# Optimization experiments

Hardware: AMD Instinct MI355X
Metric: run time of the kernel (lower is better)

Reference implementation:

```python
import jax, jax.numpy as jnp
import numpy as np

NUM_PRIMARY_CAPS = 32
PRIMARY_CAP_DIM = 8
CLASS_CAP_DIM = 16
NUM_SLOTS = 100
ROUTING_ITERS = 3
PRIOR_STRENGTH = 0.1
PRIOR_DECAY = 0.02
TEMPERATURE_INIT = 30.0

INPUT_DIM = 20000
NUM_LABELS = 100
BATCH = 4096


def _layernorm(x, g, b, eps=1e-5):
    mu = x.mean(axis=-1, keepdims=True)
    var = x.var(axis=-1, keepdims=True)
    return (x - mu) / jnp.sqrt(var + eps) * g + b


def _squash(t, axis=-1):
    sq = (t ** 2).sum(axis=axis, keepdims=True)
    scale = sq / (1.0 + sq)
    return scale * t / jnp.sqrt(sq + 1e-8)


def _l2norm(x, axis=-1, eps=1e-12):
    n = jnp.sqrt((x ** 2).sum(axis=axis, keepdims=True))
    return x / jnp.maximum(n, eps)


def setup_inputs() -> dict:
    key = jax.random.key(0)
    ks = jax.random.split(key, 12)
    features = jax.random.normal(ks[0], (BATCH, INPUT_DIM), dtype=jnp.float32)
    features = _l2norm(features)  # L2-normalised TF-IDF per docstring
    slot_features = jax.random.normal(ks[1], (BATCH, NUM_SLOTS), dtype=jnp.float32)
    # embedding MLP: Linear(input_dim,512) ReLU Linear(512,256) ReLU LayerNorm(256)
    W1 = jax.random.normal(ks[2], (INPUT_DIM, 512), dtype=jnp.float32) * 0.02
    b1 = jnp.zeros((512,), jnp.float32)
    W2 = jax.random.normal(ks[3], (512, 256), dtype=jnp.float32) * 0.05
    b2 = jnp.zeros((256,), jnp.float32)
    ln_g = jnp.ones((256,), jnp.float32)
    ln_b = jnp.zeros((256,), jnp.float32)
    # primary caps: 32 independent Linear(256,8)+LayerNorm(8), stacked
    pc_W = jax.random.normal(ks[4], (NUM_PRIMARY_CAPS, 256, PRIMARY_CAP_DIM), dtype=jnp.float32) * 0.06
    pc_b = jnp.zeros((NUM_PRIMARY_CAPS, PRIMARY_CAP_DIM), jnp.float32)
    pc_g = jnp.ones((NUM_PRIMARY_CAPS, PRIMARY_CAP_DIM), jnp.float32)
    pc_beta = jnp.zeros((NUM_PRIMARY_CAPS, PRIMARY_CAP_DIM), jnp.float32)
    # digit caps routing weights [N, K, out, in] * 0.1 per torch init
    dc_W = jax.random.normal(ks[5], (NUM_PRIMARY_CAPS, NUM_LABELS, CLASS_CAP_DIM, PRIMARY_CAP_DIM), dtype=jnp.float32) * 0.1
    slot_priors = jax.random.normal(ks[6], (NUM_SLOTS, NUM_LABELS), dtype=jnp.float32) * 0.05
    targets = _l2norm(jax.random.normal(ks[7], (NUM_LABELS, CLASS_CAP_DIM), dtype=jnp.float32))
    temperature = jnp.asarray(TEMPERATURE_INIT, dtype=jnp.float32)
    return {"features": features, "slot_features": slot_features,
            "W1": W1, "b1": b1, "W2": W2, "b2": b2, "ln_g": ln_g, "ln_b": ln_b,
            "pc_W": pc_W, "pc_b": pc_b, "pc_g": pc_g, "pc_beta": pc_beta,
            "dc_W": dc_W, "slot_priors": slot_priors, "targets": targets,
            "temperature": temperature}


def reference(features, slot_features, W1, b1, W2, b2, ln_g, ln_b,
              pc_W, pc_b, pc_g, pc_beta, dc_W, slot_priors, targets, temperature):
    # embedding MLP (dropout is identity at inference)
    h = jax.nn.relu(features @ W1 + b1)
    h = jax.nn.relu(h @ W2 + b2)
    h = _layernorm(h, ln_g, ln_b)                      # [B, 256]
    # primary capsules: [B, N=32, 8]
    prim = jnp.einsum('bc,ncd->bnd', h, pc_W) + pc_b[None]
    prim = _layernorm(prim, pc_g[None], pc_beta[None])
    # routing predictions: [B, N, K, out]
    predictions = jnp.einsum('bni,njoi->bnjo', prim, dc_W)
    B = features.shape[0]
    # slot prior: relu -> normalize to simplex -> center -> project to classes
    sf_relu = jax.nn.relu(slot_features)
    sf_w = sf_relu / jnp.maximum(sf_relu.sum(axis=1, keepdims=True), 1e-6)
    sf_w = sf_w - 1.0 / NUM_SLOTS
    sp = (sf_w @ slot_priors)[:, None, :, None]        # [B, 1, K, 1]
    b = jnp.zeros((B, NUM_PRIMARY_CAPS, predictions.shape[2], 1), predictions.dtype)
    b = b + sp * PRIOR_STRENGTH
    v = None
    for i in range(ROUTING_ITERS):
        c = jax.nn.softmax(b, axis=2)                  # coupling coefficients
        s = (predictions * c).sum(axis=1, keepdims=True)
        v = _squash(s, axis=-1)                        # [B, 1, K, out]
        if i < ROUTING_ITERS - 1:
            b = b + (predictions * v).sum(axis=-1, keepdims=True)
            strength_i = max(0.0, PRIOR_STRENGTH - PRIOR_DECAY * (i + 1))
            b = b + sp * strength_i
    class_caps = v[:, 0]                               # [B, K, out]
    caps_n = _l2norm(class_caps)
    logits = (caps_n * targets[None]).sum(axis=-1) * temperature
    return logits
```

## Files before the change

### kernel.cpp

```cpp
#include <hip/hip_runtime.h>
#include <hip/hip_bf16.h>

#define B_SZ   4096
#define NPC    32
#define NJ     100
#define CD     16
#define PD     8

typedef float  f32x4  __attribute__((ext_vector_type(4)));
typedef __bf16 bf16x8 __attribute__((ext_vector_type(8)));

__device__ __forceinline__ unsigned short f2bfr(float f) {
    union { float f; unsigned u; } v; v.f = f;
    return (unsigned short)((v.u + 0x8000u) >> 16);
}
__device__ __forceinline__ float bf_lo(unsigned u) {
    union { unsigned u; float f; } v; v.u = u << 16; return v.f;
}
__device__ __forceinline__ float bf_hi(unsigned u) {
    union { unsigned u; float f; } v; v.u = u & 0xffff0000u; return v.f;
}

__global__ __launch_bounds__(256) void transpose_cvt(
    const float* __restrict__ W, unsigned short* __restrict__ out)
{
    __shared__ float tile[32][33];
    const int kb = blockIdx.x * 32;
    const int nb = blockIdx.y * 32;
    const int tx = threadIdx.x & 31, ty = threadIdx.x >> 5;
#pragma unroll
    for (int i = 0; i < 4; ++i)
        tile[ty + 8 * i][tx] = W[(size_t)(kb + ty + 8 * i) * 512 + nb + tx];
    __syncthreads();
#pragma unroll
    for (int i = 0; i < 4; ++i)
        out[(size_t)(nb + ty + 8 * i) * 20000 + kb + tx] = f2bfr(tile[tx][ty + 8 * i]);
}

__global__ __launch_bounds__(256) void gemm1_mfma(
    const float* __restrict__ A,
    const unsigned short* __restrict__ Bt,
    float* __restrict__ C)
{
    __shared__ __align__(16) unsigned short As[128 * 32];
    __shared__ __align__(16) unsigned short Bs[128 * 32];
    const int t = threadIdx.x;
    const int lane = t & 63, w = t >> 6;
    const int id = blockIdx.x;
    const int m0 = (id & 31) * 128;
    const int n0 = ((id >> 5) & 3) * 128;
    const int z  = id >> 7;

    const int srow = t >> 2, skc = t & 3;
    const float*          Ap  = A  + (size_t)(m0 + srow) * 20000 + z * 4000 + skc * 8;
    const float*          Ap2 = Ap + (size_t)64 * 20000;
    const unsigned short* Bp  = Bt + (size_t)(n0 + srow) * 20000 + z * 4000 + skc * 8;
    const unsigned short* Bp2 = Bp + (size_t)64 * 20000;

    const int wr = w >> 1, wc = w & 1;
    const int fr = lane & 15, fq = lane >> 4;

    f32x4 acc[4][4] = {};

    for (int kt = 0; kt < 125; ++kt) {
        const int k0 = kt * 32;
        float4 a0 = *(const float4*)(Ap  + k0);
        float4 a1 = *(const float4*)(Ap  + k0 + 4);
        float4 a2 = *(const float4*)(Ap2 + k0);
        float4 a3 = *(const float4*)(Ap2 + k0 + 4);
        uint4  q0 = *(const uint4*)(Bp  + k0);
        uint4  q1 = *(const uint4*)(Bp2 + k0);
        uint4 p0, p1;
        p0.x = (unsigned)f2bfr(a0.x) | ((unsigned)f2bfr(a0.y) << 16);
        p0.y = (unsigned)f2bfr(a0.z) | ((unsigned)f2bfr(a0.w) << 16);
        p0.z = (unsigned)f2bfr(a1.x) | ((unsigned)f2bfr(a1.y) << 16);
        p0.w = (unsigned)f2bfr(a1.z) | ((unsigned)f2bfr(a1.w) << 16);
        p1.x = (unsigned)f2bfr(a2.x) | ((unsigned)f2bfr(a2.y) << 16);
        p1.y = (unsigned)f2bfr(a2.z) | ((unsigned)f2bfr(a2.w) << 16);
        p1.z = (unsigned)f2bfr(a3.x) | ((unsigned)f2bfr(a3.y) << 16);
        p1.w = (unsigned)f2bfr(a3.z) | ((unsigned)f2bfr(a3.w) << 16);
        *(uint4*)(As + (size_t)t * 8)         = p0;
        *(uint4*)(As + (size_t)(t + 256) * 8) = p1;
        *(uint4*)(Bs + (size_t)t * 8)         = q0;
        *(uint4*)(Bs + (size_t)(t + 256) * 8) = q1;
        __syncthreads();
        bf16x8 af[4], bg[4];
#pragma unroll
        for (int mi = 0; mi < 4; ++mi)
            af[mi] = *(const bf16x8*)(As + (size_t)((wr * 64 + mi * 16 + fr) * 32 + fq * 8));
#pragma unroll
        for (int ni = 0; ni < 4; ++ni)
            bg[ni] = *(const bf16x8*)(Bs + (size_t)((wc * 64 + ni * 16 + fr) * 32 + fq * 8));
#pragma unroll
        for (int mi = 0; mi < 4; ++mi)
#pragma unroll
            for (int ni = 0; ni < 4; ++ni)
                acc[mi][ni] = __builtin_amdgcn_mfma_f32_16x16x32_bf16(
                    af[mi], bg[ni], acc[mi][ni], 0, 0, 0);
        __syncthreads();
    }

    const int er = fq * 4, ec = fr;
#pragma unroll
    for (int mi = 0; mi < 4; ++mi)
#pragma unroll
    for (int ni = 0; ni < 4; ++ni) {
        const size_t base = (size_t)(m0 + wr * 64 + mi * 16 + er) * 512
                          + n0 + wc * 64 + ni * 16 + ec;
#pragma unroll
        for (int r = 0; r < 4; ++r)
            atomicAdd(&C[base + (size_t)r * 512], acc[mi][ni][r]);
    }
}

__global__ __launch_bounds__(256) void gemm2_fused(
    const float* __restrict__ A, const float* __restrict__ b1v,
    const float* __restrict__ Bm, const float* __restrict__ bias,
    float* __restrict__ C, int M, int N, int K)
{
    __shared__ float As[16][68];
    __shared__ float Bs[16][64];
    const int t  = threadIdx.x;
    const int tx = t & 15, ty = t >> 4;
    const int m0 = blockIdx.y * 64, n0 = blockIdx.x * 64;

    const int arow = t >> 2;
    const int ak   = (t & 3) << 2;
    const int bk   = t >> 4;
    const int bn   = (t & 15) << 2;

    const float* Aptr = A + (size_t)(m0 + arow) * K + ak;
    const float* Bptr = Bm + (size_t)bk * N + n0 + bn;

    float acc[4][4] = {};

    for (int k0 = 0; k0 < K; k0 += 16) {
        float4 av  = *(const float4*)(Aptr + k0);
        float4 b1q = *(const float4*)(b1v + k0 + ak);
        av.x = fmaxf(av.x + b1q.x, 0.f);
        av.y = fmaxf(av.y + b1q.y, 0.f);
        av.z = fmaxf(av.z + b1q.z, 0.f);
        av.w = fmaxf(av.w + b1q.w, 0.f);
        float4 bv = *(const float4*)(Bptr + (size_t)k0 * N);
        As[ak + 0][arow] = av.x;
        As[ak + 1][arow] = av.y;
        As[ak + 2][arow] = av.z;
        As[ak + 3][arow] = av.w;
        *(float4*)&Bs[bk][bn] = bv;
        __syncthreads();
#pragma unroll
        for (int kk = 0; kk < 16; ++kk) {
            float4 a = *(const float4*)&As[kk][ty << 2];
            float4 b = *(const float4*)&Bs[kk][tx << 2];
            acc[0][0] += a.x * b.x; acc[0][1] += a.x * b.y; acc[0][2] += a.x * b.z; acc[0][3] += a.x * b.w;
            acc[1][0] += a.y * b.x; acc[1][1] += a.y * b.y; acc[1][2] += a.y * b.z; acc[1][3] += a.y * b.w;
            acc[2][0] += a.z * b.x; acc[2][1] += a.z * b.y; acc[2][2] += a.z * b.z; acc[2][3] += a.z * b.w;
            acc[3][0] += a.w * b.x; acc[3][1] += a.w * b.y; acc[3][2] += a.w * b.z; acc[3][3] += a.w * b.w;
        }
        __syncthreads();
    }

    float4 bb = *(const float4*)(bias + n0 + (tx << 2));
#pragma unroll
    for (int i = 0; i < 4; ++i) {
        size_t m = (size_t)m0 + (ty << 2) + i;
        float4 o;
        o.x = fmaxf(acc[i][0] + bb.x, 0.f);
        o.y = fmaxf(acc[i][1] + bb.y, 0.f);
        o.z = fmaxf(acc[i][2] + bb.z, 0.f);
        o.w = fmaxf(acc[i][3] + bb.w, 0.f);
        *(float4*)(C + m * N + n0 + (tx << 2)) = o;
    }
}

__global__ __launch_bounds__(256) void layernorm256(
    const float* __restrict__ x, const float* __restrict__ g,
    const float* __restrict__ bta, float* __restrict__ y)
{
    const int w = threadIdx.x >> 6, lane = threadIdx.x & 63;
    const size_t row = (size_t)blockIdx.x * 4 + w;
    const float* xr = x + row * 256;
    float4 v = *(const float4*)(xr + lane * 4);
    float s  = v.x + v.y + v.z + v.w;
    float s2 = v.x * v.x + v.y * v.y + v.z * v.z + v.w * v.w;
#pragma unroll
    for (int off = 32; off; off >>= 1) {
        s  += __shfl_down(s, off);
        s2 += __shfl_down(s2, off);
    }
    s  = __shfl(s, 0);
    s2 = __shfl(s2, 0);
    float mu   = s * (1.f / 256.f);
    float var  = s2 * (1.f / 256.f) - mu * mu;
    float rstd = rsqrtf(var + 1e-5f);
    float4 gg = *(const float4*)(g + lane * 4);
    float4 bb = *(const float4*)(bta + lane * 4);
    float4 o;
    o.x = (v.x - mu) * rstd * gg.x + bb.x;
    o.y = (v.y - mu) * rstd * gg.y + bb.y;
    o.z = (v.z - mu) * rstd * gg.z + bb.z;
    o.w = (v.w - mu) * rstd * gg.w + bb.w;
    *(float4*)(y + row * 256 + lane * 4) = o;
}

__global__ __launch_bounds__(256) void prim_caps(
    const float* __restrict__ h, const float* __restrict__ pcW,
    const float* __restrict__ pcB, const float* __restrict__ pcG,
    const float* __restrict__ pcBeta, float* __restrict__ prim)
{
    __shared__ float hs[256];
    __shared__ float tmp[256];
    const int t = threadIdx.x;
    const size_t b = blockIdx.x;
    hs[t] = h[b * 256 + t];
    __syncthreads();
    const int n = t >> 3, d = t & 7;
    const float* wp = pcW + n * 256 * 8 + d;
    float acc = pcB[t];
#pragma unroll 4
    for (int k = 0; k < 256; ++k) acc += hs[k] * wp[k * 8];
    tmp[t] = acc;
    __syncthreads();
    float mu = 0.f, s2 = 0.f;
    const int base = n << 3;
#pragma unroll
    for (int q = 0; q < 8; ++q) {
        float xx = tmp[base + q];
        mu += xx;
        s2 += xx * xx;
    }
    mu *= 0.125f;
    s2 = s2 * 0.125f - mu * mu;
    float rstd = rsqrtf(s2 + 1e-5f);
    prim[b * 256 + t] = (acc - mu) * rstd * pcG[t] + pcBeta[t];
}

__global__ __launch_bounds__(1024, 4) void routing_b1(
    const float* __restrict__ prim,
    const float* __restrict__ sf,
    const float* __restrict__ priors,
    const float* __restrict__ dcW,
    const float* __restrict__ targets,
    const float* __restrict__ temp_p,
    float* __restrict__ out)
{
    __shared__ float    prim1[256];
    __shared__ unsigned predp[NPC * NJ * 9];
    __shared__ float    bst[NPC * NJ];
    __shared__ float    cst[NPC * NJ];
    __shared__ float    svv[NJ * 18];
    __shared__ float    spv[NJ];
    __shared__ float    rmv[NPC], irsv[NPC];
    __shared__ float    red[512];
    __shared__ float    red2[400];
    __shared__ float    ssum;

    const int t = threadIdx.x;
    const int lane = t & 63, w = t >> 6;

    const size_t b = blockIdx.x;

    if (t < 256) prim1[t] = prim[b * 256 + t];
    if (t < 128) red[t] = (t < 100) ? fmaxf(sf[b * 100 + t], 0.f) : 0.f;
    __syncthreads();

    if (t < 128) {
        float v = red[t];
#pragma unroll
        for (int d = 32; d; d >>= 1) v += __shfl_xor(v, d);
        if (lane == 0) red[128 + w] = v;
    }
    __syncthreads();
    if (t == 0) ssum = fmaxf(red[128] + red[129], 1e-6f);
    __syncthreads();

    if (t < 400) {
        const int j = t % 100, q = t / 100;
        const float inv = 1.f / ssum;
        float acc = 0.f;
#pragma unroll 5
        for (int k = q * 25; k < q * 25 + 25; ++k)
            acc += (red[k] * inv - 0.01f) * priors[k * 100 + j];
        red2[t] = acc;
    }
    __syncthreads();
    if (t < 100) spv[t] = red2[t] + red2[100 + t] + red2[200 + t] + red2[300 + t];
    __syncthreads();

    for (int r = t; r < NPC * NJ; r += 1024) bst[r] = spv[r % 100] * 0.1f;

    {
        const int c32 = lane & 31;
        const int hw  = t >> 5;
        const int ih  = (c32 & 1) * 4;
#pragma unroll 4
        for (int iter = 0; iter < 100; ++iter) {
            const int p = iter * 32 + hw;
            const int n = p / 100;
            const float4 wv = *(const float4*)(dcW + (size_t)p * 128 + c32 * 4);
            const float* pb = &prim1[n * 8 + ih];
            float part = wv.x * pb[0] + wv.y * pb[1] + wv.z * pb[2] + wv.w * pb[3];
            float po  = part + __shfl_xor(part, 1);
            float po2 = __shfl_xor(po, 2);
            if ((c32 & 3) == 0)
                predp[p * 9 + (c32 >> 2)] =
                    (unsigned)f2bfr(po) | ((unsigned)f2bfr(po2) << 16);
        }
    }
    __syncthreads();

    for (int it = 0; it < 3; ++it) {
        {
            const int n = t >> 5, q = t & 31;
            float mx = -1e30f;
            for (int j = q; j < 100; j += 32) mx = fmaxf(mx, bst[n * 100 + j]);
#pragma unroll
            for (int d = 1; d < 32; d <<= 1) mx = fmaxf(mx, __shfl_xor(mx, d));
            float se = 0.f;
            for (int j = q; j < 100; j += 32) se += __expf(bst[n * 100 + j] - mx);
#pragma unroll
            for (int d = 1; d < 32; d <<= 1) se += __shfl_xor(se, d);
            if (q == 0) { rmv[n] = mx; irsv[n] = 1.f / se; }
        }
        __syncthreads();
        for (int r = t; r < NPC * NJ; r += 1024)
            cst[r] = __expf(bst[r] - rmv[r / 100]) * irsv[r / 100];
        __syncthreads();

        if (t < 800) {
            const int j = t >> 3, op = t & 7;
            float s0 = 0.f, s1 = 0.f;
#pragma unroll
            for (int n = 0; n < NPC; ++n) {
                const float c = cst[n * 100 + j];
                const unsigned pk = predp[(n * 100 + j) * 9 + op];
                s0 += c * bf_lo(pk);
                s1 += c * bf_hi(pk);
            }
            float sq = s0 * s0 + s1 * s1;
            sq += __shfl_xor(sq, 1);
            sq += __shfl_xor(sq, 2);
            sq += __shfl_xor(sq, 4);
            const float fv = (sq / (1.f + sq)) / sqrtf(sq + 1e-8f);
            svv[j * 18 + op * 2]     = fv * s0;
            svv[j * 18 + op * 2 + 1] = fv * s1;
        }
        __syncthreads();

        if (it < 2) {
            const float str = 0.1f - 0.02f * (float)(it + 1);
            for (int r = t; r < NPC * NJ; r += 1024) {
                const int j = r % 100;
                float a = 0.f;
#pragma unroll
                for (int op = 0; op < 8; ++op) {
                    const unsigned pk = predp[r * 9 + op];
                    const float2 vv = *(const float2*)&svv[j * 18 + op * 2];
                    a += bf_lo(pk) * vv.x + bf_hi(pk) * vv.y;
                }
                bst[r] += a + spv[j] * str;
            }
            __syncthreads();
        }
    }

    if (t < 100) {
        const float T = *temp_p;
        float sq = 0.f, lg = 0.f;
#pragma unroll
        for (int o = 0; o < CD; ++o) {
            const float v = svv[t * 18 + o];
            sq += v * v;
            lg += v * targets[t * CD + o];
        }
        out[b * 100 + t] = lg * T / fmaxf(sqrtf(sq), 1e-12f);
    }
}

extern "C" void kernel_launch(void* const* d_in, const int* in_sizes, int n_in,
                              void* d_out, int out_size, void* d_ws, size_t ws_size,
                              hipStream_t stream)
{
    const float* features      = (const float*)d_in[0];
    const float* slot_features = (const float*)d_in[1];
    const float* W1            = (const float*)d_in[2];
    const float* b1            = (const float*)d_in[3];
    const float* W2            = (const float*)d_in[4];
    const float* b2            = (const float*)d_in[5];
    const float* ln_g          = (const float*)d_in[6];
    const float* ln_b          = (const float*)d_in[7];
    const float* pc_W          = (const float*)d_in[8];
    const float* pc_b          = (const float*)d_in[9];
    const float* pc_g          = (const float*)d_in[10];
    const float* pc_beta       = (const float*)d_in[11];
    const float* dc_W          = (const float*)d_in[12];
    const float* slot_priors   = (const float*)d_in[13];
    const float* targets       = (const float*)d_in[14];
    const float* temperature   = (const float*)d_in[15];
    float* out = (float*)d_out;

    unsigned short* Bt = (unsigned short*)d_ws;
    float* h1 = (float*)((char*)d_ws + (size_t)512 * 20000 * 2);
    float* h2 = h1 + (size_t)B_SZ * 512;
    float* h  = h2 + (size_t)B_SZ * 256;
    float* pr = h  + (size_t)B_SZ * 256;

    hipMemsetAsync(h1, 0, (size_t)B_SZ * 512 * sizeof(float), stream);

    transpose_cvt<<<dim3(625, 16), 256, 0, stream>>>(W1, Bt);
    gemm1_mfma<<<640, 256, 0, stream>>>(features, Bt, h1);
    gemm2_fused<<<dim3(256 / 64, B_SZ / 64), 256, 0, stream>>>(
        h1, b1, W2, b2, h2, B_SZ, 256, 512);
    layernorm256<<<B_SZ / 4, 256, 0, stream>>>(h2, ln_g, ln_b, h);
    prim_caps<<<B_SZ, 256, 0, stream>>>(h, pc_W, pc_b, pc_g, pc_beta, pr);
    routing_b1<<<B_SZ, 1024, 0, stream>>>(
        pr, slot_features, slot_priors, dc_W, targets, temperature, out);
}
```

Before: 1.362 ms.

## Fuse layernorm into primary caps, convert routing weights to bf16, remap GEMM blocks

Merges the LayerNorm and primary-capsule kernels into one per-row kernel that reads a pre-transposed pc_W for coalesced access. Pre-converts dc_W to bf16 so each routing block reads half the weight bytes when building predictions, using one thread per output pair instead of shuffle reductions. It also remaps gemm1 block indices so blocks sharing A rows are scheduled together, halves gemm2's M tile to launch more blocks, and uses packed float2 math in the routing loops. It adds two small conversion kernels per call and rounds dc_W to bf16, which slightly lowers precision.

```diff
diff --git a/kernel.cpp b/kernel.cpp
--- a/kernel.cpp
+++ b/kernel.cpp
@@ -8,6 +8,7 @@
 #define PD     8
 
 typedef float  f32x4  __attribute__((ext_vector_type(4)));
+typedef float  f32x2  __attribute__((ext_vector_type(2)));
 typedef __bf16 bf16x8 __attribute__((ext_vector_type(8)));
 
 __device__ __forceinline__ unsigned short f2bfr(float f) {
@@ -35,6 +36,29 @@
 #pragma unroll
     for (int i = 0; i < 4; ++i)
         out[(size_t)(nb + ty + 8 * i) * 20000 + kb + tx] = f2bfr(tile[tx][ty + 8 * i]);
+}
+
+__global__ __launch_bounds__(256) void cvt_dcw(
+    const float* __restrict__ W, unsigned short* __restrict__ out)
+{
+    const size_t i = ((size_t)blockIdx.x * 256 + threadIdx.x) * 8;
+    float4 f0 = *(const float4*)(W + i);
+    float4 f1 = *(const float4*)(W + i + 4);
+    uint4 o;
+    o.x = (unsigned)f2bfr(f0.x) | ((unsigned)f2bfr(f0.y) << 16);
+    o.y = (unsigned)f2bfr(f0.z) | ((unsigned)f2bfr(f0.w) << 16);
+    o.z = (unsigned)f2bfr(f1.x) | ((unsigned)f2bfr(f1.y) << 16);
+    o.w = (unsigned)f2bfr(f1.z) | ((unsigned)f2bfr(f1.w) << 16);
+    *(uint4*)(out + i) = o;
+}
+
+__global__ __launch_bounds__(256) void cvt_pcwt(
+    const float* __restrict__ W, float* __restrict__ out)
+{
+    const int idx = blockIdx.x * 256 + threadIdx.x;
+    const int k = idx >> 8, c = idx & 255;
+    const int n = c >> 3, d = c & 7;
+    out[idx] = W[(size_t)(n * 256 + k) * 8 + d];
 }
 
 __global__ __launch_bounds__(256) void gemm1_mfma(
@@ -47,9 +71,13 @@
     const int t = threadIdx.x;
     const int lane = t & 63, w = t >> 6;
     const int id = blockIdx.x;
-    const int m0 = (id & 31) * 128;
-    const int n0 = ((id >> 5) & 3) * 128;
-    const int z  = id >> 7;
+    const int x  = id & 7;
+    const int q  = id >> 3;
+    const int nb = q & 3;
+    const int g  = (q >> 2) * 8 + x;
+    const int z  = g >> 5;
+    const int m0 = (g & 31) * 128;
+    const int n0 = nb * 128;
 
     const int srow = t >> 2, skc = t & 3;
     const float*          Ap  = A  + (size_t)(m0 + srow) * 20000 + z * 4000 + skc * 8;
@@ -118,52 +146,46 @@
     const float* __restrict__ Bm, const float* __restrict__ bias,
     float* __restrict__ C, int M, int N, int K)
 {
-    __shared__ float As[16][68];
+    __shared__ float As[16][34];
     __shared__ float Bs[16][64];
     const int t  = threadIdx.x;
     const int tx = t & 15, ty = t >> 4;
-    const int m0 = blockIdx.y * 64, n0 = blockIdx.x * 64;
-
-    const int arow = t >> 2;
-    const int ak   = (t & 3) << 2;
+    const int m0 = blockIdx.y * 32, n0 = blockIdx.x * 64;
+
+    const int arow = t >> 3;
+    const int ak   = (t & 7) << 1;
     const int bk   = t >> 4;
     const int bn   = (t & 15) << 2;
 
     const float* Aptr = A + (size_t)(m0 + arow) * K + ak;
     const float* Bptr = Bm + (size_t)bk * N + n0 + bn;
 
-    float acc[4][4] = {};
+    float acc[2][4] = {};
 
     for (int k0 = 0; k0 < K; k0 += 16) {
-        float4 av  = *(const float4*)(Aptr + k0);
-        float4 b1q = *(const float4*)(b1v + k0 + ak);
+        float2 av  = *(const float2*)(Aptr + k0);
+        float2 b1q = *(const float2*)(b1v + k0 + ak);
         av.x = fmaxf(av.x + b1q.x, 0.f);
         av.y = fmaxf(av.y + b1q.y, 0.f);
-        av.z = fmaxf(av.z + b1q.z, 0.f);
-        av.w = fmaxf(av.w + b1q.w, 0.f);
         float4 bv = *(const float4*)(Bptr + (size_t)k0 * N);
         As[ak + 0][arow] = av.x;
         As[ak + 1][arow] = av.y;
-        As[ak + 2][arow] = av.z;
-        As[ak + 3][arow] = av.w;
         *(float4*)&Bs[bk][bn] = bv;
         __syncthreads();
 #pragma unroll
         for (int kk = 0; kk < 16; ++kk) {
-            float4 a = *(const float4*)&As[kk][ty << 2];
+            float2 a = *(const float2*)&As[kk][ty << 1];
             float4 b = *(const float4*)&Bs[kk][tx << 2];
             acc[0][0] += a.x * b.x; acc[0][1] += a.x * b.y; acc[0][2] += a.x * b.z; acc[0][3] += a.x * b.w;
             acc[1][0] += a.y * b.x; acc[1][1] += a.y * b.y; acc[1][2] += a.y * b.z; acc[1][3] += a.y * b.w;
-            acc[2][0] += a.z * b.x; acc[2][1] += a.z * b.y; acc[2][2] += a.z * b.z; acc[2][3] += a.z * b.w;
-            acc[3][0] += a.w * b.x; acc[3][1] += a.w * b.y; acc[3][2] += a.w * b.z; acc[3][3] += a.w * b.w;
         }
         __syncthreads();
     }
 
     float4 bb = *(const float4*)(bias + n0 + (tx << 2));
 #pragma unroll
-    for (int i = 0; i < 4; ++i) {
-        size_t m = (size_t)m0 + (ty << 2) + i;
+    for (int i = 0; i < 2; ++i) {
+        size_t m = (size_t)m0 + (ty << 1) + i;
         float4 o;
         o.x = fmaxf(acc[i][0] + bb.x, 0.f);
         o.y = fmaxf(acc[i][1] + bb.y, 0.f);
@@ -173,82 +195,71 @@
     }
 }
 
-__global__ __launch_bounds__(256) void layernorm256(
-    const float* __restrict__ x, const float* __restrict__ g,
-    const float* __restrict__ bta, float* __restrict__ y)
-{
-    const int w = threadIdx.x >> 6, lane = threadIdx.x & 63;
-    const size_t row = (size_t)blockIdx.x * 4 + w;
-    const float* xr = x + row * 256;
-    float4 v = *(const float4*)(xr + lane * 4);
-    float s  = v.x + v.y + v.z + v.w;
-    float s2 = v.x * v.x + v.y * v.y + v.z * v.z + v.w * v.w;
+__global__ __launch_bounds__(256) void ln_prim(
+    const float* __restrict__ h2, const float* __restrict__ lng,
+    const float* __restrict__ lnb, const float* __restrict__ pcWT,
+    const float* __restrict__ pcB, const float* __restrict__ pcG,
+    const float* __restrict__ pcBeta, float* __restrict__ prim)
+{
+    __shared__ float hs[256];
+    __shared__ float tmp[256];
+    __shared__ float r8[8];
+    const int t = threadIdx.x;
+    const int lane = t & 63, w = t >> 6;
+    const size_t b = blockIdx.x;
+
+    float x = h2[b * 256 + t];
+    float s = x, s2 = x * x;
 #pragma unroll
     for (int off = 32; off; off >>= 1) {
-        s  += __shfl_down(s, off);
-        s2 += __shfl_down(s2, off);
-    }
-    s  = __shfl(s, 0);
-    s2 = __shfl(s2, 0);
+        s  += __shfl_xor(s, off);
+        s2 += __shfl_xor(s2, off);
+    }
+    if (lane == 0) { r8[w] = s; r8[4 + w] = s2; }
+    __syncthreads();
+    s  = r8[0] + r8[1] + r8[2] + r8[3];
+    s2 = r8[4] + r8[5] + r8[6] + r8[7];
     float mu   = s * (1.f / 256.f);
     float var  = s2 * (1.f / 256.f) - mu * mu;
     float rstd = rsqrtf(var + 1e-5f);
-    float4 gg = *(const float4*)(g + lane * 4);
-    float4 bb = *(const float4*)(bta + lane * 4);
-    float4 o;
-    o.x = (v.x - mu) * rstd * gg.x + bb.x;
-    o.y = (v.y - mu) * rstd * gg.y + bb.y;
-    o.z = (v.z - mu) * rstd * gg.z + bb.z;
-    o.w = (v.w - mu) * rstd * gg.w + bb.w;
-    *(float4*)(y + row * 256 + lane * 4) = o;
-}
-
-__global__ __launch_bounds__(256) void prim_caps(
-    const float* __restrict__ h, const float* __restrict__ pcW,
-    const float* __restrict__ pcB, const float* __restrict__ pcG,
-    const float* __restrict__ pcBeta, float* __restrict__ prim)
-{
-    __shared__ float hs[256];
-    __shared__ float tmp[256];
-    const int t = threadIdx.x;
-    const size_t b = blockIdx.x;
-    hs[t] = h[b * 256 + t];
-    __syncthreads();
-    const int n = t >> 3, d = t & 7;
-    const float* wp = pcW + n * 256 * 8 + d;
+    hs[t] = (x - mu) * rstd * lng[t] + lnb[t];
+    __syncthreads();
+
     float acc = pcB[t];
 #pragma unroll 4
-    for (int k = 0; k < 256; ++k) acc += hs[k] * wp[k * 8];
+    for (int k = 0; k < 256; ++k) acc += hs[k] * pcWT[k * 256 + t];
     tmp[t] = acc;
     __syncthreads();
-    float mu = 0.f, s2 = 0.f;
+
+    const int n = t >> 3;
+    float cmu = 0.f, cs2 = 0.f;
     const int base = n << 3;
 #pragma unroll
-    for (int q = 0; q < 8; ++q) {
-        float xx = tmp[base + q];
-        mu += xx;
-        s2 += xx * xx;
-    }
-    mu *= 0.125f;
-    s2 = s2 * 0.125f - mu * mu;
-    float rstd = rsqrtf(s2 + 1e-5f);
-    prim[b * 256 + t] = (acc - mu) * rstd * pcG[t] + pcBeta[t];
+    for (int qq = 0; qq < 8; ++qq) {
+        float xx = tmp[base + qq];
+        cmu += xx;
+        cs2 += xx * xx;
+    }
+    cmu *= 0.125f;
+    cs2 = cs2 * 0.125f - cmu * cmu;
+    float crstd = rsqrtf(cs2 + 1e-5f);
+    prim[b * 256 + t] = (acc - cmu) * crstd * pcG[t] + pcBeta[t];
 }
 
 __global__ __launch_bounds__(1024, 4) void routing_b1(
     const float* __restrict__ prim,
     const float* __restrict__ sf,
     const float* __restrict__ priors,
-    const float* __restrict__ dcW,
+    const unsigned short* __restrict__ dcWb,
     const float* __restrict__ targets,
     const float* __restrict__ temp_p,
     float* __restrict__ out)
 {
-    __shared__ float    prim1[256];
+    __shared__ __align__(16) float prim1[256];
     __shared__ unsigned predp[NPC * NJ * 9];
     __shared__ float    bst[NPC * NJ];
     __shared__ float    cst[NPC * NJ];
-    __shared__ float    svv[NJ * 18];
+    __shared__ __align__(16) float svv[NJ * 18];
     __shared__ float    spv[NJ];
     __shared__ float    rmv[NPC], irsv[NPC];
     __shared__ float    red[512];
@@ -290,21 +301,27 @@
     for (int r = t; r < NPC * NJ; r += 1024) bst[r] = spv[r % 100] * 0.1f;
 
     {
-        const int c32 = lane & 31;
-        const int hw  = t >> 5;
-        const int ih  = (c32 & 1) * 4;
-#pragma unroll 4
-        for (int iter = 0; iter < 100; ++iter) {
-            const int p = iter * 32 + hw;
+        const int g8 = t >> 3;
+        const int op = t & 7;
+        const unsigned short* wp0 = dcWb + (size_t)g8 * 128 + op * 16;
+#pragma unroll 5
+        for (int iter = 0; iter < 25; ++iter) {
+            const int p = iter * 128 + g8;
             const int n = p / 100;
-            const float4 wv = *(const float4*)(dcW + (size_t)p * 128 + c32 * 4);
-            const float* pb = &prim1[n * 8 + ih];
-            float part = wv.x * pb[0] + wv.y * pb[1] + wv.z * pb[2] + wv.w * pb[3];
-            float po  = part + __shfl_xor(part, 1);
-            float po2 = __shfl_xor(po, 2);
-            if ((c32 & 3) == 0)
-                predp[p * 9 + (c32 >> 2)] =
-                    (unsigned)f2bfr(po) | ((unsigned)f2bfr(po2) << 16);
+            const uint4 w0 = *(const uint4*)(wp0 + (size_t)iter * 16384);
+            const uint4 w1 = *(const uint4*)(wp0 + (size_t)iter * 16384 + 8);
+            const float4 pa = *(const float4*)&prim1[n * 8];
+            const float4 pb = *(const float4*)&prim1[n * 8 + 4];
+            float po  = bf_lo(w0.x) * pa.x + bf_hi(w0.x) * pa.y
+                      + bf_lo(w0.y) * pa.z + bf_hi(w0.y) * pa.w
+                      + bf_lo(w0.z) * pb.x + bf_hi(w0.z) * pb.y
+                      + bf_lo(w0.w) * pb.z + bf_hi(w0.w) * pb.w;
+            float po2 = bf_lo(w1.x) * pa.x + bf_hi(w1.x) * pa.y
+                      + bf_lo(w1.y) * pa.z + bf_hi(w1.y) * pa.w
+                      + bf_lo(w1.z) * pb.x + bf_hi(w1.z) * pb.y
+                      + bf_lo(w1.w) * pb.z + bf_hi(w1.w) * pb.w;
+            predp[p * 9 + op] =
+                (unsigned)f2bfr(po) | ((unsigned)f2bfr(po2) << 16);
         }
     }
     __syncthreads();
@@ -329,14 +346,16 @@
 
         if (t < 800) {
             const int j = t >> 3, op = t & 7;
-            float s0 = 0.f, s1 = 0.f;
+            f32x2 acc2 = {0.f, 0.f};
 #pragma unroll
             for (int n = 0; n < NPC; ++n) {
                 const float c = cst[n * 100 + j];
                 const unsigned pk = predp[(n * 100 + j) * 9 + op];
-                s0 += c * bf_lo(pk);
-                s1 += c * bf_hi(pk);
+                f32x2 pv = {bf_lo(pk), bf_hi(pk)};
+                f32x2 c2 = {c, c};
+                acc2 += pv * c2;
             }
+            float s0 = acc2.x, s1 = acc2.y;
             float sq = s0 * s0 + s1 * s1;
             sq += __shfl_xor(sq, 1);
             sq += __shfl_xor(sq, 2);
@@ -351,14 +370,15 @@
             const float str = 0.1f - 0.02f * (float)(it + 1);
             for (int r = t; r < NPC * NJ; r += 1024) {
                 const int j = r % 100;
-                float a = 0.f;
+                f32x2 a2 = {0.f, 0.f};
 #pragma unroll
                 for (int op = 0; op < 8; ++op) {
                     const unsigned pk = predp[r * 9 + op];
-                    const float2 vv = *(const float2*)&svv[j * 18 + op * 2];
-                    a += bf_lo(pk) * vv.x + bf_hi(pk) * vv.y;
+                    const f32x2 vv = *(const f32x2*)&svv[j * 18 + op * 2];
+                    f32x2 pv = {bf_lo(pk), bf_hi(pk)};
+                    a2 += pv * vv;
                 }
-                bst[r] += a + spv[j] * str;
+                bst[r] += (a2.x + a2.y) + spv[j] * str;
             }
             __syncthreads();
         }
@@ -402,17 +422,19 @@
     unsigned short* Bt = (unsigned short*)d_ws;
     float* h1 = (float*)((char*)d_ws + (size_t)512 * 20000 * 2);
     float* h2 = h1 + (size_t)B_SZ * 512;
-    float* h  = h2 + (size_t)B_SZ * 256;
-    float* pr = h  + (size_t)B_SZ * 256;
+    float* pcWT = h2 + (size_t)B_SZ * 256;
+    float* pr = pcWT + (size_t)B_SZ * 256;
+    unsigned short* dcWb = (unsigned short*)(pr + (size_t)B_SZ * 256);
 
     hipMemsetAsync(h1, 0, (size_t)B_SZ * 512 * sizeof(float), stream);
 
     transpose_cvt<<<dim3(625, 16), 256, 0, stream>>>(W1, Bt);
+    cvt_dcw<<<200, 256, 0, stream>>>(dc_W, dcWb);
+    cvt_pcwt<<<256, 256, 0, stream>>>(pc_W, pcWT);
     gemm1_mfma<<<640, 256, 0, stream>>>(features, Bt, h1);
-    gemm2_fused<<<dim3(256 / 64, B_SZ / 64), 256, 0, stream>>>(
+    gemm2_fused<<<dim3(256 / 64, B_SZ / 32), 256, 0, stream>>>(
         h1, b1, W2, b2, h2, B_SZ, 256, 512);
-    layernorm256<<<B_SZ / 4, 256, 0, stream>>>(h2, ln_g, ln_b, h);
-    prim_caps<<<B_SZ, 256, 0, stream>>>(h, pc_W, pc_b, pc_g, pc_beta, pr);
+    ln_prim<<<B_SZ, 256, 0, stream>>>(h2, ln_g, ln_b, pcWT, pc_b, pc_g, pc_beta, pr);
     routing_b1<<<B_SZ, 1024, 0, stream>>>(
-        pr, slot_features, slot_priors, dc_W, targets, temperature, out);
-}
+        pr, slot_features, slot_priors, dcWb, targets, temperature, out);
+}
```

After: 1.114 ms. 18.2% less time.
